# Optimization experiments

Measured on AMD Instinct MI355X. Metric: run time of the kernel, lower is better.

Reference implementation:

```python
import jax, jax.numpy as jnp
import numpy as np

B, T, N = 1024, 1024, 32


def setup_inputs() -> dict:
    key = jax.random.key(0)
    k1, k2, k3 = jax.random.split(key, 3)
    logits = jax.random.normal(k1, (B, T, N), dtype=jnp.float32)
    transitions = jax.random.normal(k2, (N, N), dtype=jnp.float32) * 0.1
    sequence_lengths = jax.random.randint(k3, (B,), 0, T, dtype=jnp.int32)
    return {"logits": logits, "transitions": transitions, "sequence_lengths": sequence_lengths}


def reference(logits, transitions, sequence_lengths):
    # Viterbi decode (tfa.text.crf.crf_decode), then mask padding positions to 0.
    Bd, Td, Nd = logits.shape
    tag_ids = jnp.arange(Nd, dtype=jnp.int32)
    init_state = logits[:, 0, :]  # [B, N] viterbi scores at t=0

    def step(state, xs):
        logit_t, t = xs
        # scores[b, prev, cur] = state[b, prev] + transitions[prev, cur]
        scores = state[:, :, None] + transitions[None, :, :]  # [B, N, N]
        bp = jnp.argmax(scores, axis=1).astype(jnp.int32)      # [B, N] best prev tag
        new_state = jnp.max(scores, axis=1) + logit_t          # [B, N]
        valid = (t < sequence_lengths)[:, None]                # step t valid if t <= len-1
        state = jnp.where(valid, new_state, state)             # freeze state past seq end
        bp = jnp.where(valid, bp, tag_ids[None, :])            # identity backptr past end
        return state, bp

    xs = (jnp.swapaxes(logits[:, 1:, :], 0, 1), jnp.arange(1, Td))
    final_state, bps = jax.lax.scan(step, init_state, xs)      # bps: [T-1, B, N]
    last_tag = jnp.argmax(final_state, axis=-1).astype(jnp.int32)  # [B]

    def back(tag, bp):
        prev = jnp.take_along_axis(bp, tag[:, None], axis=1)[:, 0]
        return prev, tag  # emit tag at position i+1, carry tag at position i

    first_tag, later = jax.lax.scan(back, last_tag, bps, reverse=True)
    pred = jnp.concatenate([first_tag[:, None], jnp.swapaxes(later, 0, 1)], axis=1)  # [B, T]
    mask = (jnp.arange(Td)[None, :] < sequence_lengths[:, None]).astype(pred.dtype)
    return pred * mask
```

## Files before the change

kernel.cpp:

```cpp
#include <hip/hip_runtime.h>
#include <stdint.h>

#define T_LEN 1024
#define NSTATE 32

typedef int v2i __attribute__((ext_vector_type(2)));

__device__ __forceinline__ float max3f(float a, float b, float c) {
    return fmaxf(fmaxf(a, b), c);
}
__device__ __forceinline__ int min3i(int a, int b, int c) {
    return min(min(a, b), c);
}

#define ROR(x, n) __builtin_amdgcn_mov_dpp((x), 0x120 + (n), 0xF, 0xF, false)

__device__ __forceinline__ void gather16(int x, int g[16]) {
    g[0]  = x;
    g[1]  = ROR(g[0], 1);
    g[2]  = ROR(g[0], 2);
    g[3]  = ROR(g[1], 2);
    g[4]  = ROR(g[0], 4);
    g[5]  = ROR(g[1], 4);
    g[6]  = ROR(g[2], 4);
    g[7]  = ROR(g[3], 4);
    g[8]  = ROR(g[0], 8);
    g[9]  = ROR(g[1], 8);
    g[10] = ROR(g[2], 8);
    g[11] = ROR(g[3], 8);
    g[12] = ROR(g[4], 8);
    g[13] = ROR(g[5], 8);
    g[14] = ROR(g[6], 8);
    g[15] = ROR(g[7], 8);
}

__device__ __forceinline__ int xrow16_partner(int own) {
    int a = own, b = own;
#if __has_builtin(__builtin_amdgcn_permlane16_swap)
    v2i r = __builtin_amdgcn_permlane16_swap(a, b, false, false);
    a = r[0]; b = r[1];
#else
    asm volatile("v_permlane16_swap_b32 %0, %1" : "+v"(a), "+v"(b));
#endif
    return (a == own) ? b : a;
}

__launch_bounds__(64)
__global__ void viterbi_kernel(const float* __restrict__ logits,
                               const float* __restrict__ trans,
                               const int* __restrict__ seqlen,
                               int* __restrict__ out)
{
    const int lane = threadIdx.x;
    const int j    = lane & 31;
    const int myidx = (lane < 32) ? j : (j ^ 16);
    const bool upper = lane >= 32;

    __shared__ uint8_t bp[T_LEN * NSTATE];
    __shared__ uint8_t Farr[NSTATE * NSTATE];
    __shared__ uint8_t earr[NSTATE];
    __shared__ __align__(16) int pred[T_LEN];

    int L = seqlen[blockIdx.x];
    L = min(max(L, 0), T_LEN);

    int pidx[16];
    gather16(myidx, pidx);

    float tr_rot[16];
#pragma unroll
    for (int k = 0; k < 16; ++k)
        tr_rot[k] = trans[pidx[k] * NSTATE + j];

    const float* lg = logits + (size_t)blockIdx.x * T_LEN * NSTATE;

    float ns = lg[myidx];

    auto step = [&](int t, float lgt) {
        int gb[16];
        gather16(__float_as_int(ns), gb);

        float v[16];
#pragma unroll
        for (int k = 0; k < 16; ++k)
            v[k] = __int_as_float(gb[k]) + tr_rot[k];

        float a0 = max3f(v[0],  v[1],  v[2]);
        float a1 = max3f(v[3],  v[4],  v[5]);
        float a2 = max3f(v[6],  v[7],  v[8]);
        float a3 = max3f(v[9],  v[10], v[11]);
        float a4 = max3f(v[12], v[13], v[14]);
        float b0 = max3f(a0, a1, a2);
        float b1 = max3f(a3, a4, v[15]);
        float hm = fmaxf(b0, b1);

        v2i sw = __builtin_amdgcn_permlane32_swap(__float_as_int(hm),
                                                  __float_as_int(hm), false, false);
        float gm = fmaxf(hm, fmaxf(__int_as_float(sw[0]), __int_as_float(sw[1])));

        ns = gm + lgt;

        int ix[16];
#pragma unroll
        for (int k = 0; k < 16; ++k)
            ix[k] = (v[k] == gm) ? pidx[k] : 64;
        int c0 = min3i(ix[0],  ix[1],  ix[2]);
        int c1 = min3i(ix[3],  ix[4],  ix[5]);
        int c2 = min3i(ix[6],  ix[7],  ix[8]);
        int c3 = min3i(ix[9],  ix[10], ix[11]);
        int c4 = min3i(ix[12], ix[13], ix[14]);
        int d0 = min3i(c0, c1, c2);
        int d1 = min3i(c3, c4, ix[15]);
        int ih = min(d0, d1);
        v2i swi = __builtin_amdgcn_permlane32_swap(ih, ih, false, false);
        int idx = min(ih, min(swi[0], swi[1]));

        bp[t * NSTATE + j] = (uint8_t)idx;

        int part = xrow16_partner(__float_as_int(ns));
        if (upper) ns = __int_as_float(part);
    };

    if (L >= 2) {
        float pre[8];
#pragma unroll
        for (int d = 0; d < 8; ++d) {
            int tp = 1 + d; if (tp > 1023) tp = 1023;
            pre[d] = lg[tp * NSTATE + j];
        }
        for (int t = 1; t < L; t += 8) {
#pragma unroll
            for (int u = 0; u < 8; ++u) {
                if (t + u < L)
                    step(t + u, pre[u]);
                int tp = t + 8 + u; if (tp > 1023) tp = 1023;
                pre[u] = lg[tp * NSTATE + j];
            }
        }
    }

    float m = ns;
#pragma unroll
    for (int d = 1; d < 64; d <<= 1) m = fmaxf(m, __shfl_xor(m, d));
    int ii = (ns == m) ? myidx : 64;
#pragma unroll
    for (int d = 1; d < 64; d <<= 1) ii = min(ii, __shfl_xor(ii, d));
    const int ft = ii;

    __syncthreads();

    {
        const int c = lane & 31;
        const int j0base = (lane >> 5) * 16;
        int tags[16];
#pragma unroll
        for (int k = 0; k < 16; ++k) tags[k] = j0base + k;
        const int thi = c * 32 + 31;
        for (int s = 0; s < 32; ++s) {
            int t = thi - s;
            bool valid = (t >= 1) && (t <= L - 1);
            int tc = min(max(t, 1), max(L - 1, 1));
            int base = tc * NSTATE;
#pragma unroll
            for (int k = 0; k < 16; ++k) {
                int nt = bp[base + tags[k]];
                tags[k] = valid ? nt : tags[k];
            }
        }
#pragma unroll
        for (int k = 0; k < 16; ++k)
            Farr[c * 32 + j0base + k] = (uint8_t)tags[k];
    }
    __syncthreads();

    if (lane == 0) {
        int e = ft;
        for (int c2 = 31; c2 >= 0; --c2) {
            earr[c2] = (uint8_t)e;
            e = Farr[c2 * 32 + e];
        }
    }
    __syncthreads();

    if (lane < 32) {
        int tag = earr[lane];
        const int thi3 = lane * 32 + 31;
        for (int s = 0; s < 32; ++s) {
            int t = thi3 - s;
            pred[t] = (t < L) ? tag : 0;
            bool valid = (t >= 1) && (t <= L - 1);
            int tc = min(max(t, 1), max(L - 1, 1));
            int nt = bp[tc * NSTATE + tag];
            tag = valid ? nt : tag;
        }
    }
    __syncthreads();

    int4* out4 = reinterpret_cast<int4*>(out + (size_t)blockIdx.x * T_LEN);
    const int4* p4 = reinterpret_cast<const int4*>(pred);
#pragma unroll
    for (int r = 0; r < 4; ++r)
        out4[r * 64 + lane] = p4[r * 64 + lane];
}

extern "C" void kernel_launch(void* const* d_in, const int* in_sizes, int n_in,
                              void* d_out, int out_size, void* d_ws, size_t ws_size,
                              hipStream_t stream) {
    const float* logits = (const float*)d_in[0];
    const float* trans  = (const float*)d_in[1];
    const int*   slen   = (const int*)d_in[2];
    int*         out    = (int*)d_out;
    const int B = in_sizes[2];

    viterbi_kernel<<<dim3(B), dim3(64), 0, stream>>>(logits, trans, slen, out);
}
```

Baseline: 282.4 us.

## Double-buffer logits prefetch with explicit vmcnt waits and branchless predicated steps

Splits the logits prefetch into two 8-step register buffers, issuing the loads for one buffer while the other is consumed. Explicit s_waitcnt calls with sched barriers wait only for the older batch of loads instead of a full drain. Each step now runs unconditionally with a select-based activity flag, so the inner branch goes away and the loop is padded to a multiple of 16. Padded steps write into an extra bp row, at the cost of extra wasted steps past the sequence end and more register use.

```diff
diff --git a/kernel.cpp b/kernel.cpp
--- a/kernel.cpp
+++ b/kernel.cpp
@@ -45,6 +45,9 @@
     return (a == own) ? b : a;
 }
 
+#define WAIT_VM8() do { __builtin_amdgcn_s_waitcnt(0xF78); \
+                        __builtin_amdgcn_sched_barrier(0); } while (0)
+
 __launch_bounds__(64)
 __global__ void viterbi_kernel(const float* __restrict__ logits,
                                const float* __restrict__ trans,
@@ -56,7 +59,7 @@
     const int myidx = (lane < 32) ? j : (j ^ 16);
     const bool upper = lane >= 32;
 
-    __shared__ uint8_t bp[T_LEN * NSTATE];
+    __shared__ uint8_t bp[(T_LEN + 1) * NSTATE];
     __shared__ uint8_t Farr[NSTATE * NSTATE];
     __shared__ uint8_t earr[NSTATE];
     __shared__ __align__(16) int pred[T_LEN];
@@ -76,7 +79,7 @@
 
     float ns = lg[myidx];
 
-    auto step = [&](int t, float lgt) {
+    auto step = [&](int t, float lgt, bool act) {
         int gb[16];
         gather16(__float_as_int(ns), gb);
 
@@ -98,7 +101,8 @@
                                                   __float_as_int(hm), false, false);
         float gm = fmaxf(hm, fmaxf(__int_as_float(sw[0]), __int_as_float(sw[1])));
 
-        ns = gm + lgt;
+        float nsn = gm + lgt;
+        float ns_sel = act ? nsn : ns;
 
         int ix[16];
 #pragma unroll
@@ -113,28 +117,49 @@
         int d1 = min3i(c3, c4, ix[15]);
         int ih = min(d0, d1);
         v2i swi = __builtin_amdgcn_permlane32_swap(ih, ih, false, false);
-        int idx = min(ih, min(swi[0], swi[1]));
-
-        bp[t * NSTATE + j] = (uint8_t)idx;
-
-        int part = xrow16_partner(__float_as_int(ns));
-        if (upper) ns = __int_as_float(part);
+        int idx = min3i(ih, swi[0], swi[1]);
+
+        int tc = min(t, T_LEN);
+        bp[tc * NSTATE + j] = (uint8_t)idx;
+
+        int part = xrow16_partner(__float_as_int(ns_sel));
+        ns = (upper && act) ? __int_as_float(part) : ns_sel;
     };
 
-    if (L >= 2) {
-        float pre[8];
-#pragma unroll
-        for (int d = 0; d < 8; ++d) {
-            int tp = 1 + d; if (tp > 1023) tp = 1023;
-            pre[d] = lg[tp * NSTATE + j];
-        }
-        for (int t = 1; t < L; t += 8) {
+    {
+        const int steps = max(L - 1, 0);
+        const int P = (steps + 15) & ~15;
+
+        float preA[8], preB[8];
+#pragma unroll
+        for (int u = 0; u < 8; ++u) {
+            int tp = min(1 + u, T_LEN - 1);
+            preA[u] = lg[tp * NSTATE + j];
+        }
+#pragma unroll
+        for (int u = 0; u < 8; ++u) {
+            int tp = min(9 + u, T_LEN - 1);
+            preB[u] = lg[tp * NSTATE + j];
+        }
+
+        for (int t = 1; t + 15 <= P; t += 16) {
+            WAIT_VM8();
+#pragma unroll
+            for (int u = 0; u < 8; ++u)
+                step(t + u, preA[u], (t + u) < L);
 #pragma unroll
             for (int u = 0; u < 8; ++u) {
-                if (t + u < L)
-                    step(t + u, pre[u]);
-                int tp = t + 8 + u; if (tp > 1023) tp = 1023;
-                pre[u] = lg[tp * NSTATE + j];
+                int tp = min(t + 16 + u, T_LEN - 1);
+                preA[u] = lg[tp * NSTATE + j];
+            }
+            WAIT_VM8();
+#pragma unroll
+            for (int u = 0; u < 8; ++u)
+                step(t + 8 + u, preB[u], (t + 8 + u) < L);
+#pragma unroll
+            for (int u = 0; u < 8; ++u) {
+                int tp = min(t + 24 + u, T_LEN - 1);
+                preB[u] = lg[tp * NSTATE + j];
             }
         }
     }
```

Result: faster. 261.7 us (-7.4%).
